# Performance work log

Measured on AMD Instinct MI355X. Metric: run time of the kernel, lower is better.

## Reference

```python
import jax, jax.numpy as jnp
import numpy as np

DIM = 256
HEAD_DIM = 32
HEADS = DIM // HEAD_DIM
SHAPE = (64, 64)          # (H, W) patch grid
WS = 8                    # window size
SHIFT = 4                 # shift size (ws // 2)
SCALE = HEAD_DIM ** -0.5
WS2 = WS * WS


def _rel_indices(ws):
    # relative position index for every (query, key) pair in a window
    a = np.arange(ws)
    y1, x1, y2, x2 = np.meshgrid(a, a, a, a, indexing='ij')
    idx = (y1 - y2 + ws - 1) * (2 * ws - 1) + (x1 - x2 + ws - 1)
    return idx.reshape(ws * ws, ws * ws)  # (ws2, ws2)


def _shift_mask(shape, ws, shift):
    # region labels per patch, 9 regions from the 3x3 slice grid
    H, W = shape
    region = np.zeros((H, W), dtype=np.int32)
    slices = [slice(0, -ws), slice(-ws, -shift), slice(-shift, None)]
    num = 0
    for i in slices:
        for j in slices:
            region[i, j] = num
            num += 1
    # window-partition the region map -> (n_windows, ws2)
    nH, nW = H // ws, W // ws
    r = region.reshape(nH, ws, nW, ws).transpose(0, 2, 1, 3).reshape(nH * nW, ws * ws)
    # True where query and key come from different regions
    return (r[:, None, :] - r[:, :, None]) != 0  # (nw, ws2, ws2)


REL_IDX = jnp.asarray(_rel_indices(WS))                 # (ws2, ws2) int
MASK = jnp.asarray(_shift_mask(SHAPE, WS, SHIFT))       # (nw, ws2, ws2) bool


def _split_windows(x, ws):
    # (b, H, W, C) -> (b * nH * nW, ws*ws, C)
    b, H, W, C = x.shape
    x = x.reshape(b, H // ws, ws, W // ws, ws, C)
    x = x.transpose(0, 1, 3, 2, 4, 5)
    return x.reshape(-1, ws * ws, C)


def _merge_windows(x, shape, ws):
    # inverse of _split_windows
    H, W = shape
    nH, nW = H // ws, W // ws
    C = x.shape[-1]
    x = x.reshape(-1, nH, nW, ws, ws, C)
    x = x.transpose(0, 1, 3, 2, 4, 5)
    return x.reshape(-1, H, W, C)


def setup_inputs() -> dict:
    key = jax.random.key(0)
    ks = jax.random.split(key, 6)
    s = 0.02
    return {
        'x': jax.random.normal(ks[0], (32, SHAPE[0] * SHAPE[1], DIM), jnp.float32),
        'w_qkv': jax.random.normal(ks[1], (3 * DIM, DIM), jnp.float32) * s,
        'b_qkv': jax.random.normal(ks[2], (3 * DIM,), jnp.float32) * s,
        'w_out': jax.random.normal(ks[3], (DIM, DIM), jnp.float32) * s,
        'b_out': jax.random.normal(ks[4], (DIM,), jnp.float32) * s,
        'pos_enc': jax.random.normal(ks[5], (HEADS, (2 * WS - 1) ** 2), jnp.float32) * s,
    }


def reference(x, w_qkv, b_qkv, w_out, b_out, pos_enc):
    B, N, C = x.shape
    H, W = SHAPE
    nw = (H // WS) * (W // WS)

    xg = x.reshape(B, H, W, C)
    if SHIFT > 0:
        xg = jnp.roll(xg, (-SHIFT, -SHIFT), axis=(1, 2))
    xw = _split_windows(xg, WS)                        # (B*nw, ws2, C)

    qkv = xw @ w_qkv.T + b_qkv                         # (B*nw, ws2, 3C)
    qkv = qkv.reshape(-1, WS2, 3, HEADS, HEAD_DIM)
    q, k, v = (qkv[:, :, i].transpose(0, 2, 1, 3) for i in range(3))  # (Bn, h, ws2, hd)

    attn = jnp.einsum('bhqd,bhkd->bhqk', q, k) * SCALE  # (Bn, h, ws2, ws2)
    bias = pos_enc[:, REL_IDX]                          # (h, ws2, ws2)
    attn = attn + bias[None]

    if SHIFT > 0:
        attn = attn.reshape(B, nw, HEADS, WS2, WS2)
        attn = jnp.where(MASK[None, :, None], -jnp.inf, attn)
        attn = attn.reshape(B * nw, HEADS, WS2, WS2)

    attn = jax.nn.softmax(attn, axis=-1)
    out = jnp.einsum('bhqk,bhkd->bhqd', attn, v)        # (Bn, h, ws2, hd)
    out = out.transpose(0, 2, 1, 3).reshape(-1, WS2, C)
    out = out @ w_out.T + b_out                         # (Bn, ws2, C)

    out = _merge_windows(out, SHAPE, WS)                # (B, H, W, C)
    if SHIFT > 0:
        out = jnp.roll(out, (SHIFT, SHIFT), axis=(1, 2))
    return out.reshape(B, N, C)
```

## Files before the change

kernel.cpp:

```cpp
#include <hip/hip_runtime.h>
#include <stdint.h>


typedef short short8 __attribute__((ext_vector_type(8)));
typedef float f32x4 __attribute__((ext_vector_type(4)));

typedef __attribute__((address_space(1))) uint32_t g_u32;
typedef __attribute__((address_space(3))) uint32_t l_u32;

#define SCALE 0.17677669529663687f

__device__ __forceinline__ uint16_t f2bf(float f) {
  union { float f; uint32_t u; } c; c.f = f;
  uint32_t r = c.u + 0x7FFFu + ((c.u >> 16) & 1u);
  return (uint16_t)(r >> 16);
}

__device__ __forceinline__ void g2lds16(const void* g, void* l) {
  __builtin_amdgcn_global_load_lds((const g_u32*)g, (l_u32*)l, 16, 0, 0);
}

__global__ __launch_bounds__(256) void cvtx_kernel(const float* __restrict__ x,
                                                   uint16_t* __restrict__ xb) {
  int tid = threadIdx.x;
  int token = blockIdx.x * 8 + (tid >> 5);
  int c = (tid & 31) * 8;
  int w = token >> 6, t = token & 63;
  int b = w >> 6, wd = w & 63;
  int h = (wd >> 3) * 8 + (t >> 3);
  int xx = (wd & 7) * 8 + (t & 7);
  int src = b * 4096 + (((h + 4) & 63) << 6) + ((xx + 4) & 63);
  const float* sp = x + (size_t)src * 256 + c;
  f32x4 a = *(const f32x4*)sp;
  f32x4 d = *(const f32x4*)(sp + 4);
  short8 v;
  v[0] = (short)f2bf(a[0]); v[1] = (short)f2bf(a[1]);
  v[2] = (short)f2bf(a[2]); v[3] = (short)f2bf(a[3]);
  v[4] = (short)f2bf(d[0]); v[5] = (short)f2bf(d[1]);
  v[6] = (short)f2bf(d[2]); v[7] = (short)f2bf(d[3]);
  *(short8*)&xb[(size_t)token * 256 + c] = v;
}

__global__ __launch_bounds__(256) void cvt_kernel(const float* __restrict__ in,
                                                  uint16_t* __restrict__ out, int n) {
  int i = (blockIdx.x * 256 + threadIdx.x) * 8;
  if (i >= n) return;
  f32x4 a = *(const f32x4*)(in + i);
  f32x4 b = *(const f32x4*)(in + i + 4);
  short8 v;
  v[0] = (short)f2bf(a[0]); v[1] = (short)f2bf(a[1]);
  v[2] = (short)f2bf(a[2]); v[3] = (short)f2bf(a[3]);
  v[4] = (short)f2bf(b[0]); v[5] = (short)f2bf(b[1]);
  v[6] = (short)f2bf(b[2]); v[7] = (short)f2bf(b[3]);
  *(short8*)(out + i) = v;
}

__global__ __launch_bounds__(256) void bias_kernel(const float* __restrict__ pe,
                                                   float* __restrict__ bm) {
  int bx = blockIdx.x;
  int wd = bx >> 3, head = bx & 7;
  int hw = wd >> 3, ww = wd & 7;
  int tid = threadIdx.x;
  int kk = tid >> 2, a0 = (tid & 3) * 4;
  int jy = kk >> 3, jx = kk & 7;
  int hj = hw * 8 + jy, xj = ww * 8 + jx;
  int rj = (hj >= 60 ? 2 : (hj >= 56 ? 1 : 0)) * 3 + (xj >= 60 ? 2 : (xj >= 56 ? 1 : 0));
  float* dst = bm + (size_t)bx * 4096 + kk * 64 + a0 * 4;
  for (int aa = 0; aa < 4; ++aa) {
    int a = a0 + aa;
    f32x4 v;
#pragma unroll
    for (int ni = 0; ni < 4; ++ni) {
      int i = ni * 16 + a;
      int iy = i >> 3, ix = i & 7;
      int hi = hw * 8 + iy, xi = ww * 8 + ix;
      int ri = (hi >= 60 ? 2 : (hi >= 56 ? 1 : 0)) * 3 + (xi >= 60 ? 2 : (xi >= 56 ? 1 : 0));
      v[ni] = (ri != rj) ? -1e30f : pe[head * 225 + (iy - jy + 7) * 15 + (ix - jx + 7)];
    }
    *(f32x4*)(dst + aa * 4) = v;
  }
}

__global__ __launch_bounds__(256) void qkv_kernel(
    const uint16_t* __restrict__ xb, const uint16_t* __restrict__ wq,
    const float* __restrict__ bqkv,
    uint16_t* __restrict__ qws, uint16_t* __restrict__ kws, uint16_t* __restrict__ vws) {
  __shared__ uint16_t sm[16384];
  uint16_t* As = sm;
  uint16_t* Bs = sm + 4096;
  const int tid = threadIdx.x, lane = tid & 63, wv = tid >> 6;
  const int quad = lane >> 4, l15 = lane & 15;
  const int n0 = blockIdx.x * 128;
  const int m0 = blockIdx.y * 128;

  const int c0 = wv * 2, c1 = c0 + 1;
  const uint16_t* ap0 = xb + (size_t)(m0 + c0 * 16 + (lane >> 2)) * 256 + (lane & 3) * 8;
  const uint16_t* ap1 = xb + (size_t)(m0 + c1 * 16 + (lane >> 2)) * 256 + (lane & 3) * 8;
  const uint16_t* bp0 = wq + (size_t)(n0 + c0 * 16 + (lane >> 2)) * 256 + (lane & 3) * 8;
  const uint16_t* bp1 = wq + (size_t)(n0 + c1 * 16 + (lane >> 2)) * 256 + (lane & 3) * 8;

  const int wm = (wv & 1) * 64, wn = (wv >> 1) * 64;
  f32x4 zero = {0.f, 0.f, 0.f, 0.f};
  f32x4 acc[4][4];
#pragma unroll
  for (int mi = 0; mi < 4; ++mi)
#pragma unroll
    for (int ni = 0; ni < 4; ++ni) acc[mi][ni] = zero;

  for (int ks = 0; ks < 8; ++ks) {
    int k0 = ks * 32;
    g2lds16(ap0 + k0, &As[c0 * 512]);
    g2lds16(ap1 + k0, &As[c1 * 512]);
    g2lds16(bp0 + k0, &Bs[c0 * 512]);
    g2lds16(bp1 + k0, &Bs[c1 * 512]);
    __syncthreads();
    short8 af[4], bf[4];
#pragma unroll
    for (int mi = 0; mi < 4; ++mi)
      af[mi] = *(const short8*)&As[(wm + mi * 16 + l15) * 32 + quad * 8];
#pragma unroll
    for (int ni = 0; ni < 4; ++ni)
      bf[ni] = *(const short8*)&Bs[(wn + ni * 16 + l15) * 32 + quad * 8];
#pragma unroll
    for (int mi = 0; mi < 4; ++mi)
#pragma unroll
      for (int ni = 0; ni < 4; ++ni)
        acc[mi][ni] = __builtin_amdgcn_mfma_f32_16x16x32_bf16(af[mi], bf[ni], acc[mi][ni], 0, 0, 0);
    __syncthreads();
  }

  float bq4[4];
#pragma unroll
  for (int ni = 0; ni < 4; ++ni) bq4[ni] = bqkv[n0 + wn + ni * 16 + l15];
  const int ng0 = n0 + wn;
  const int sct = ng0 >> 8;
  uint16_t* epi = sm + wv * 4096;

  if (sct < 2) {
#pragma unroll
    for (int mi = 0; mi < 4; ++mi)
#pragma unroll
      for (int ni = 0; ni < 4; ++ni)
#pragma unroll
        for (int r = 0; r < 4; ++r) {
          int t = mi * 16 + quad * 4 + r, n = ni * 16 + l15;
          epi[t * 64 + ((((n >> 3) ^ (t & 7)) << 3) | (n & 7))] = f2bf(acc[mi][ni][r] + bq4[ni]);
        }
    uint16_t* dst = (sct == 0) ? qws : kws;
    const int tb = m0 + wm;
#pragma unroll
    for (int cc = 0; cc < 8; ++cc) {
      int chunk = cc * 64 + lane;
      int trow = chunk >> 3, part = chunk & 7;
      short8 v = *(const short8*)&epi[trow * 64 + ((part ^ (trow & 7)) << 3)];
      int tok = tb + trow, w = tok >> 6, t = tok & 63;
      int ng = ng0 + part * 8, hd = (ng >> 5) & 7, d = ng & 31;
      *(short8*)&dst[(size_t)((w * 8 + hd) * 64 + t) * 32 + d] = v;
    }
  } else {
#pragma unroll
    for (int mi = 0; mi < 4; ++mi)
#pragma unroll
      for (int ni = 0; ni < 4; ++ni)
#pragma unroll
        for (int r = 0; r < 4; ++r) {
          int t = mi * 16 + quad * 4 + r, n = ni * 16 + l15;
          epi[n * 64 + ((((t >> 3) ^ (n & 7)) << 3) | (t & 7))] = f2bf(acc[mi][ni][r] + bq4[ni]);
        }
    const int tb = m0 + wm;
#pragma unroll
    for (int cc = 0; cc < 8; ++cc) {
      int chunk = cc * 64 + lane;
      int drow = chunk >> 3, part = chunk & 7;
      short8 v = *(const short8*)&epi[drow * 64 + ((part ^ (drow & 7)) << 3)];
      int ng = ng0 + drow, hd = (ng >> 5) & 7, d = ng & 31;
      int tok = tb + part * 8, w = tok >> 6, t = tok & 63;
      *(short8*)&vws[(size_t)((w * 8 + hd) * 32 + d) * 64 + t] = v;
    }
  }
}

__global__ __launch_bounds__(256) void attn_kernel(
    const uint16_t* __restrict__ qws, const uint16_t* __restrict__ kws,
    const uint16_t* __restrict__ vws, const float* __restrict__ bm,
    uint16_t* __restrict__ ao) {
  __shared__ uint16_t P[4][4096];
  const int tid = threadIdx.x, lane = tid & 63, wv = tid >> 6;
  const int quad = lane >> 4, l15 = lane & 15;
  const int gid = blockIdx.x * 4 + wv;
  const int w = gid >> 3, head = gid & 7;
  const uint16_t* qb = qws + (size_t)(w * 8 + head) * 2048;
  const uint16_t* kb = kws + (size_t)(w * 8 + head) * 2048;
  const uint16_t* vb = vws + (size_t)(w * 8 + head) * 2048;
  const float* bmh = bm + (size_t)((w & 63) * 8 + head) * 4096;
  f32x4 zero = {0.f, 0.f, 0.f, 0.f};

  short8 ak[4], bq[4];
#pragma unroll
  for (int mi = 0; mi < 4; ++mi)
    ak[mi] = *(const short8*)&kb[(mi * 16 + l15) * 32 + quad * 8];
#pragma unroll
  for (int ni = 0; ni < 4; ++ni)
    bq[ni] = *(const short8*)&qb[(ni * 16 + l15) * 32 + quad * 8];

  f32x4 s[4][4];
#pragma unroll
  for (int mi = 0; mi < 4; ++mi)
#pragma unroll
    for (int ni = 0; ni < 4; ++ni)
      s[mi][ni] = __builtin_amdgcn_mfma_f32_16x16x32_bf16(ak[mi], bq[ni], zero, 0, 0, 0);

#pragma unroll
  for (int mi = 0; mi < 4; ++mi)
#pragma unroll
    for (int r = 0; r < 4; ++r) {
      int kk = mi * 16 + quad * 4 + r;
      f32x4 b4 = *(const f32x4*)&bmh[kk * 64 + l15 * 4];
#pragma unroll
      for (int ni = 0; ni < 4; ++ni)
        s[mi][ni][r] = s[mi][ni][r] * SCALE + b4[ni];
    }

#pragma unroll
  for (int ni = 0; ni < 4; ++ni) {
    float mx = s[0][ni][0];
#pragma unroll
    for (int mi = 0; mi < 4; ++mi)
#pragma unroll
      for (int r = 0; r < 4; ++r) mx = fmaxf(mx, s[mi][ni][r]);
    mx = fmaxf(mx, __shfl_xor(mx, 16, 64));
    mx = fmaxf(mx, __shfl_xor(mx, 32, 64));
    float sum = 0.f;
#pragma unroll
    for (int mi = 0; mi < 4; ++mi)
#pragma unroll
      for (int r = 0; r < 4; ++r) {
        float e = __expf(s[mi][ni][r] - mx);
        s[mi][ni][r] = e;
        sum += e;
      }
    sum += __shfl_xor(sum, 16, 64);
    sum += __shfl_xor(sum, 32, 64);
    float inv = 1.f / sum;
#pragma unroll
    for (int mi = 0; mi < 4; ++mi)
#pragma unroll
      for (int r = 0; r < 4; ++r) s[mi][ni][r] *= inv;
  }

  uint16_t* Pw = P[wv];
#pragma unroll
  for (int mi = 0; mi < 4; ++mi)
#pragma unroll
    for (int ni = 0; ni < 4; ++ni)
#pragma unroll
      for (int rp = 0; rp < 2; ++rp) {
        int kk = mi * 16 + quad * 4 + rp * 2;
        int q = ni * 16 + l15;
        uint32_t pk = (uint32_t)f2bf(s[mi][ni][rp * 2]) |
                      ((uint32_t)f2bf(s[mi][ni][rp * 2 + 1]) << 16);
        *(uint32_t*)&Pw[q * 64 + ((((kk >> 3) ^ (q & 7)) << 3) | (kk & 7))] = pk;
      }

  f32x4 o[4][2];
#pragma unroll
  for (int mi = 0; mi < 4; ++mi) { o[mi][0] = zero; o[mi][1] = zero; }
#pragma unroll
  for (int ki = 0; ki < 2; ++ki) {
    short8 vf0 = *(const short8*)&vb[(l15) * 64 + ki * 32 + quad * 8];
    short8 vf1 = *(const short8*)&vb[(16 + l15) * 64 + ki * 32 + quad * 8];
#pragma unroll
    for (int mi = 0; mi < 4; ++mi) {
      int q = mi * 16 + l15;
      short8 pa = *(const short8*)&Pw[q * 64 + (((ki * 4 + quad) ^ (q & 7)) << 3)];
      o[mi][0] = __builtin_amdgcn_mfma_f32_16x16x32_bf16(pa, vf0, o[mi][0], 0, 0, 0);
      o[mi][1] = __builtin_amdgcn_mfma_f32_16x16x32_bf16(pa, vf1, o[mi][1], 0, 0, 0);
    }
  }
#pragma unroll
  for (int mi = 0; mi < 4; ++mi)
#pragma unroll
    for (int ni = 0; ni < 2; ++ni)
#pragma unroll
      for (int r = 0; r < 4; ++r) {
        int t = mi * 16 + quad * 4 + r;
        ao[(size_t)(w * 64 + t) * 256 + head * 32 + ni * 16 + l15] = f2bf(o[mi][ni][r]);
      }
}

__global__ __launch_bounds__(256) void oproj_kernel(
    const uint16_t* __restrict__ aob, const uint16_t* __restrict__ wo,
    const float* __restrict__ bout, float* __restrict__ out) {
  __shared__ uint16_t sm[8192];
  uint16_t* As = sm;
  uint16_t* Bs = sm + 4096;
  const int tid = threadIdx.x, lane = tid & 63, wv = tid >> 6;
  const int quad = lane >> 4, l15 = lane & 15;
  const int n0 = blockIdx.x * 128;
  const int m0 = blockIdx.y * 128;

  const int c0 = wv * 2, c1 = c0 + 1;
  const uint16_t* ap0 = aob + (size_t)(m0 + c0 * 16 + (lane >> 2)) * 256 + (lane & 3) * 8;
  const uint16_t* ap1 = aob + (size_t)(m0 + c1 * 16 + (lane >> 2)) * 256 + (lane & 3) * 8;
  const uint16_t* bp0 = wo + (size_t)(n0 + c0 * 16 + (lane >> 2)) * 256 + (lane & 3) * 8;
  const uint16_t* bp1 = wo + (size_t)(n0 + c1 * 16 + (lane >> 2)) * 256 + (lane & 3) * 8;

  const int wm = (wv & 1) * 64, wn = (wv >> 1) * 64;
  f32x4 zero = {0.f, 0.f, 0.f, 0.f};
  f32x4 acc[4][4];
#pragma unroll
  for (int mi = 0; mi < 4; ++mi)
#pragma unroll
    for (int ni = 0; ni < 4; ++ni) acc[mi][ni] = zero;

  for (int ks = 0; ks < 8; ++ks) {
    int k0 = ks * 32;
    g2lds16(ap0 + k0, &As[c0 * 512]);
    g2lds16(ap1 + k0, &As[c1 * 512]);
    g2lds16(bp0 + k0, &Bs[c0 * 512]);
    g2lds16(bp1 + k0, &Bs[c1 * 512]);
    __syncthreads();
    short8 af[4], bf[4];
#pragma unroll
    for (int mi = 0; mi < 4; ++mi)
      af[mi] = *(const short8*)&As[(wm + mi * 16 + l15) * 32 + quad * 8];
#pragma unroll
    for (int ni = 0; ni < 4; ++ni)
      bf[ni] = *(const short8*)&Bs[(wn + ni * 16 + l15) * 32 + quad * 8];
#pragma unroll
    for (int mi = 0; mi < 4; ++mi)
#pragma unroll
      for (int ni = 0; ni < 4; ++ni)
        acc[mi][ni] = __builtin_amdgcn_mfma_f32_16x16x32_bf16(af[mi], bf[ni], acc[mi][ni], 0, 0, 0);
    __syncthreads();
  }

  float bo4[4];
#pragma unroll
  for (int ni = 0; ni < 4; ++ni) bo4[ni] = bout[n0 + wn + ni * 16 + l15];
#pragma unroll
  for (int mi = 0; mi < 4; ++mi) {
    int mb = m0 + wm + mi * 16 + quad * 4;
    int w = mb >> 6, t0 = mb & 63;
    int b = w >> 6, wd = w & 63;
    int hw2 = wd >> 3, ww2 = wd & 7;
#pragma unroll
    for (int r = 0; r < 4; ++r) {
      int t = t0 + r;
      int h = hw2 * 8 + (t >> 3), xx = ww2 * 8 + (t & 7);
      int row = (((h + 4) & 63) << 6) | ((xx + 4) & 63);
      float* op = out + ((size_t)b * 4096 + row) * 256 + n0 + wn;
#pragma unroll
      for (int ni = 0; ni < 4; ++ni) op[ni * 16 + l15] = acc[mi][ni][r] + bo4[ni];
    }
  }
}

extern "C" void kernel_launch(void* const* d_in, const int* in_sizes, int n_in,
                              void* d_out, int out_size, void* d_ws, size_t ws_size,
                              hipStream_t stream) {
  const float* x = (const float*)d_in[0];
  const float* w_qkv = (const float*)d_in[1];
  const float* b_qkv = (const float*)d_in[2];
  const float* w_out = (const float*)d_in[3];
  const float* b_out = (const float*)d_in[4];
  const float* pos_enc = (const float*)d_in[5];
  float* out = (float*)d_out;

  uint8_t* ws = (uint8_t*)d_ws;
  uint16_t* xb  = (uint16_t*)(ws);
  uint16_t* wqb = (uint16_t*)(ws + 67108864);
  uint16_t* wob = (uint16_t*)(ws + 67502080);
  float*    bmt = (float*)   (ws + 67633152);
  uint16_t* qws = (uint16_t*)(ws + 76021760);
  uint16_t* kws = (uint16_t*)(ws + 143130624);
  uint16_t* vws = (uint16_t*)(ws + 210239488);
  uint16_t* aob = xb;

  cvtx_kernel<<<16384, 256, 0, stream>>>(x, xb);
  cvt_kernel<<<96, 256, 0, stream>>>(w_qkv, wqb, 196608);
  cvt_kernel<<<32, 256, 0, stream>>>(w_out, wob, 65536);
  bias_kernel<<<512, 256, 0, stream>>>(pos_enc, bmt);
  qkv_kernel<<<dim3(6, 1024), 256, 0, stream>>>(xb, wqb, b_qkv, qws, kws, vws);
  attn_kernel<<<4096, 256, 0, stream>>>(qws, kws, vws, bmt, aob);
  oproj_kernel<<<dim3(2, 1024), 256, 0, stream>>>(aob, wob, b_out, out);
}
```

Baseline: 446.4 us.

## Fuse x shift/convert into QKV GEMM with resident A tile and swizzled LDS

The separate fp32-to-bf16 shifted-window conversion pass over x is removed. The QKV kernel now loads its 128-token fp32 slice directly, converts it and keeps the full 128x256 bf16 A tile resident in LDS, then loops over all six 128-column output tiles with double-buffered weight loads. The two weight conversion launches are merged into one, and XOR swizzling is added to the LDS layout in both GEMMs to reduce bank conflicts. In exchange the kernel uses much more LDS (80 KB), which limits occupancy, and the grid shrinks to 1024 blocks.

Result: faster. 394.7 us (-11.6%).

```diff
diff --git a/kernel.cpp b/kernel.cpp
--- a/kernel.cpp
+++ b/kernel.cpp
@@ -3,6 +3,7 @@
 
 
 typedef short short8 __attribute__((ext_vector_type(8)));
+typedef short s16x4 __attribute__((ext_vector_type(4)));
 typedef float f32x4 __attribute__((ext_vector_type(4)));
 
 typedef __attribute__((address_space(1))) uint32_t g_u32;
@@ -20,33 +21,13 @@
   __builtin_amdgcn_global_load_lds((const g_u32*)g, (l_u32*)l, 16, 0, 0);
 }
 
-__global__ __launch_bounds__(256) void cvtx_kernel(const float* __restrict__ x,
-                                                   uint16_t* __restrict__ xb) {
-  int tid = threadIdx.x;
-  int token = blockIdx.x * 8 + (tid >> 5);
-  int c = (tid & 31) * 8;
-  int w = token >> 6, t = token & 63;
-  int b = w >> 6, wd = w & 63;
-  int h = (wd >> 3) * 8 + (t >> 3);
-  int xx = (wd & 7) * 8 + (t & 7);
-  int src = b * 4096 + (((h + 4) & 63) << 6) + ((xx + 4) & 63);
-  const float* sp = x + (size_t)src * 256 + c;
-  f32x4 a = *(const f32x4*)sp;
-  f32x4 d = *(const f32x4*)(sp + 4);
-  short8 v;
-  v[0] = (short)f2bf(a[0]); v[1] = (short)f2bf(a[1]);
-  v[2] = (short)f2bf(a[2]); v[3] = (short)f2bf(a[3]);
-  v[4] = (short)f2bf(d[0]); v[5] = (short)f2bf(d[1]);
-  v[6] = (short)f2bf(d[2]); v[7] = (short)f2bf(d[3]);
-  *(short8*)&xb[(size_t)token * 256 + c] = v;
-}
-
-__global__ __launch_bounds__(256) void cvt_kernel(const float* __restrict__ in,
-                                                  uint16_t* __restrict__ out, int n) {
+__global__ __launch_bounds__(256) void cvtw_kernel(const float* __restrict__ wq,
+                                                   const float* __restrict__ wo,
+                                                   uint16_t* __restrict__ out) {
   int i = (blockIdx.x * 256 + threadIdx.x) * 8;
-  if (i >= n) return;
-  f32x4 a = *(const f32x4*)(in + i);
-  f32x4 b = *(const f32x4*)(in + i + 4);
+  const float* src = (i < 196608) ? (wq + i) : (wo + (i - 196608));
+  f32x4 a = *(const f32x4*)src;
+  f32x4 b = *(const f32x4*)(src + 4);
   short8 v;
   v[0] = (short)f2bf(a[0]); v[1] = (short)f2bf(a[1]);
   v[2] = (short)f2bf(a[2]); v[3] = (short)f2bf(a[3]);
@@ -81,102 +62,155 @@
   }
 }
 
-__global__ __launch_bounds__(256) void qkv_kernel(
-    const uint16_t* __restrict__ xb, const uint16_t* __restrict__ wq,
+__global__ __launch_bounds__(256, 2) void qkv_kernel(
+    const float* __restrict__ x, const uint16_t* __restrict__ wq,
     const float* __restrict__ bqkv,
     uint16_t* __restrict__ qws, uint16_t* __restrict__ kws, uint16_t* __restrict__ vws) {
-  __shared__ uint16_t sm[16384];
+  __shared__ uint16_t sm[40960];
   uint16_t* As = sm;
-  uint16_t* Bs = sm + 4096;
+  uint16_t* Bs = sm + 32768;
   const int tid = threadIdx.x, lane = tid & 63, wv = tid >> 6;
   const int quad = lane >> 4, l15 = lane & 15;
-  const int n0 = blockIdx.x * 128;
-  const int m0 = blockIdx.y * 128;
-
-  const int c0 = wv * 2, c1 = c0 + 1;
-  const uint16_t* ap0 = xb + (size_t)(m0 + c0 * 16 + (lane >> 2)) * 256 + (lane & 3) * 8;
-  const uint16_t* ap1 = xb + (size_t)(m0 + c1 * 16 + (lane >> 2)) * 256 + (lane & 3) * 8;
-  const uint16_t* bp0 = wq + (size_t)(n0 + c0 * 16 + (lane >> 2)) * 256 + (lane & 3) * 8;
-  const uint16_t* bp1 = wq + (size_t)(n0 + c1 * 16 + (lane >> 2)) * 256 + (lane & 3) * 8;
-
+  const int m0 = blockIdx.x * 128;
+
+  {
+    const int rl = tid >> 3;
+    const int cg = tid & 7;
+    for (int pass = 0; pass < 4; ++pass) {
+      int row = pass * 32 + rl;
+      int token = m0 + row;
+      int w = token >> 6, t = token & 63;
+      int b = w >> 6, wd = w & 63;
+      int h = (wd >> 3) * 8 + (t >> 3);
+      int xx = (wd & 7) * 8 + (t & 7);
+      const float* sp = x + (size_t)(b * 4096 + (((h + 4) & 63) << 6) + ((xx + 4) & 63)) * 256;
+      int psw = (row >> 1) & 3;
+#pragma unroll
+      for (int j = 0; j < 4; ++j) {
+        int c0 = cg * 8 + j * 64;
+        f32x4 a = *(const f32x4*)(sp + c0);
+        f32x4 d = *(const f32x4*)(sp + c0 + 4);
+        short8 v;
+        v[0] = (short)f2bf(a[0]); v[1] = (short)f2bf(a[1]);
+        v[2] = (short)f2bf(a[2]); v[3] = (short)f2bf(a[3]);
+        v[4] = (short)f2bf(d[0]); v[5] = (short)f2bf(d[1]);
+        v[6] = (short)f2bf(d[2]); v[7] = (short)f2bf(d[3]);
+        int ks = c0 >> 5, g = (c0 >> 3) & 3;
+        *(short8*)&As[(ks * 128 + row) * 32 + (g ^ psw) * 8] = v;
+      }
+    }
+  }
+
+  const int c0s = wv * 2, c1s = c0s + 1;
+  const int perm = ((lane & 3) ^ ((lane >> 3) & 3)) * 8;
   const int wm = (wv & 1) * 64, wn = (wv >> 1) * 64;
+  const int fsw = (quad ^ ((l15 >> 1) & 3)) * 8;
+  const int tb = m0 + wm;
+  uint16_t* epi = &Bs[wv * 2048];
   f32x4 zero = {0.f, 0.f, 0.f, 0.f};
-  f32x4 acc[4][4];
-#pragma unroll
-  for (int mi = 0; mi < 4; ++mi)
-#pragma unroll
-    for (int ni = 0; ni < 4; ++ni) acc[mi][ni] = zero;
-
-  for (int ks = 0; ks < 8; ++ks) {
-    int k0 = ks * 32;
-    g2lds16(ap0 + k0, &As[c0 * 512]);
-    g2lds16(ap1 + k0, &As[c1 * 512]);
-    g2lds16(bp0 + k0, &Bs[c0 * 512]);
-    g2lds16(bp1 + k0, &Bs[c1 * 512]);
+
+  __syncthreads();
+
+  for (int nt = 0; nt < 6; ++nt) {
+    const int n0 = nt * 128;
+    const uint16_t* bp0 = wq + (size_t)(n0 + c0s * 16 + (lane >> 2)) * 256 + perm;
+    const uint16_t* bp1 = wq + (size_t)(n0 + c1s * 16 + (lane >> 2)) * 256 + perm;
+    g2lds16(bp0, &Bs[c0s * 512]);
+    g2lds16(bp1, &Bs[c1s * 512]);
+
+    f32x4 acc[4][4];
+#pragma unroll
+    for (int mi = 0; mi < 4; ++mi)
+#pragma unroll
+      for (int ni = 0; ni < 4; ++ni) acc[mi][ni] = zero;
+
     __syncthreads();
-    short8 af[4], bf[4];
-#pragma unroll
-    for (int mi = 0; mi < 4; ++mi)
-      af[mi] = *(const short8*)&As[(wm + mi * 16 + l15) * 32 + quad * 8];
-#pragma unroll
-    for (int ni = 0; ni < 4; ++ni)
-      bf[ni] = *(const short8*)&Bs[(wn + ni * 16 + l15) * 32 + quad * 8];
-#pragma unroll
-    for (int mi = 0; mi < 4; ++mi)
+
+    for (int ks = 0; ks < 8; ++ks) {
+      int buf = (ks & 1) * 4096;
+      if (ks < 7) {
+        int nbuf = 4096 - buf;
+        g2lds16(bp0 + (ks + 1) * 32, &Bs[nbuf + c0s * 512]);
+        g2lds16(bp1 + (ks + 1) * 32, &Bs[nbuf + c1s * 512]);
+      }
+      short8 af[4], bf[4];
+#pragma unroll
+      for (int mi = 0; mi < 4; ++mi)
+        af[mi] = *(const short8*)&As[(ks * 128 + wm + mi * 16 + l15) * 32 + fsw];
 #pragma unroll
       for (int ni = 0; ni < 4; ++ni)
-        acc[mi][ni] = __builtin_amdgcn_mfma_f32_16x16x32_bf16(af[mi], bf[ni], acc[mi][ni], 0, 0, 0);
+        bf[ni] = *(const short8*)&Bs[buf + (wn + ni * 16 + l15) * 32 + fsw];
+#pragma unroll
+      for (int mi = 0; mi < 4; ++mi)
+#pragma unroll
+        for (int ni = 0; ni < 4; ++ni)
+          acc[mi][ni] = __builtin_amdgcn_mfma_f32_16x16x32_bf16(af[mi], bf[ni], acc[mi][ni], 0, 0, 0);
+      __syncthreads();
+    }
+
+    float bq4[4];
+#pragma unroll
+    for (int ni = 0; ni < 4; ++ni) bq4[ni] = bqkv[n0 + wn + ni * 16 + l15];
+    const int ng0 = n0 + wn;
+    const int sct = ng0 >> 8;
+
+    if (sct < 2) {
+      uint16_t* dst = (sct == 0) ? qws : kws;
+      for (int half = 0; half < 2; ++half) {
+#pragma unroll
+        for (int mi2 = 0; mi2 < 2; ++mi2) {
+          int mi = half * 2 + mi2;
+#pragma unroll
+          for (int ni = 0; ni < 4; ++ni)
+#pragma unroll
+            for (int r = 0; r < 4; ++r) {
+              int t = mi * 16 + quad * 4 + r, tl = t & 31;
+              int n = ni * 16 + l15;
+              epi[tl * 64 + ((((n >> 3) ^ (t & 7)) << 3) | (n & 7))] =
+                  f2bf(acc[mi][ni][r] + bq4[ni]);
+            }
+        }
+#pragma unroll
+        for (int cc = 0; cc < 4; ++cc) {
+          int chunk = cc * 64 + lane;
+          int trl = chunk >> 3, part = chunk & 7;
+          int t = half * 32 + trl;
+          short8 v = *(const short8*)&epi[trl * 64 + ((part ^ (t & 7)) << 3)];
+          int tok = tb + t, w = tok >> 6, tt = tok & 63;
+          int ng = ng0 + part * 8, hd = (ng >> 5) & 7, d = ng & 31;
+          *(short8*)&dst[(size_t)((w * 8 + hd) * 64 + tt) * 32 + d] = v;
+        }
+      }
+    } else {
+      for (int half = 0; half < 2; ++half) {
+#pragma unroll
+        for (int ni2 = 0; ni2 < 2; ++ni2) {
+          int ni = half * 2 + ni2;
+          int n = ni * 16 + l15, nl = n & 31;
+#pragma unroll
+          for (int mi = 0; mi < 4; ++mi) {
+            int t0 = mi * 16 + quad * 4;
+            s16x4 pv;
+            pv[0] = (short)f2bf(acc[mi][ni][0] + bq4[ni]);
+            pv[1] = (short)f2bf(acc[mi][ni][1] + bq4[ni]);
+            pv[2] = (short)f2bf(acc[mi][ni][2] + bq4[ni]);
+            pv[3] = (short)f2bf(acc[mi][ni][3] + bq4[ni]);
+            *(s16x4*)&epi[nl * 64 + ((((t0 >> 3) ^ (n & 7)) << 3) | (t0 & 7))] = pv;
+          }
+        }
+#pragma unroll
+        for (int cc = 0; cc < 4; ++cc) {
+          int chunk = cc * 64 + lane;
+          int drl = chunk >> 3, part = chunk & 7;
+          int dr = half * 32 + drl;
+          short8 v = *(const short8*)&epi[drl * 64 + ((part ^ (dr & 7)) << 3)];
+          int ng = ng0 + dr, hd = (ng >> 5) & 7, d = ng & 31;
+          int tok = tb + part * 8, w = tok >> 6, t = tok & 63;
+          *(short8*)&vws[(size_t)((w * 8 + hd) * 32 + d) * 64 + t] = v;
+        }
+      }
+    }
     __syncthreads();
-  }
-
-  float bq4[4];
-#pragma unroll
-  for (int ni = 0; ni < 4; ++ni) bq4[ni] = bqkv[n0 + wn + ni * 16 + l15];
-  const int ng0 = n0 + wn;
-  const int sct = ng0 >> 8;
-  uint16_t* epi = sm + wv * 4096;
-
-  if (sct < 2) {
-#pragma unroll
-    for (int mi = 0; mi < 4; ++mi)
-#pragma unroll
-      for (int ni = 0; ni < 4; ++ni)
-#pragma unroll
-        for (int r = 0; r < 4; ++r) {
-          int t = mi * 16 + quad * 4 + r, n = ni * 16 + l15;
-          epi[t * 64 + ((((n >> 3) ^ (t & 7)) << 3) | (n & 7))] = f2bf(acc[mi][ni][r] + bq4[ni]);
-        }
-    uint16_t* dst = (sct == 0) ? qws : kws;
-    const int tb = m0 + wm;
-#pragma unroll
-    for (int cc = 0; cc < 8; ++cc) {
-      int chunk = cc * 64 + lane;
-      int trow = chunk >> 3, part = chunk & 7;
-      short8 v = *(const short8*)&epi[trow * 64 + ((part ^ (trow & 7)) << 3)];
-      int tok = tb + trow, w = tok >> 6, t = tok & 63;
-      int ng = ng0 + part * 8, hd = (ng >> 5) & 7, d = ng & 31;
-      *(short8*)&dst[(size_t)((w * 8 + hd) * 64 + t) * 32 + d] = v;
-    }
-  } else {
-#pragma unroll
-    for (int mi = 0; mi < 4; ++mi)
-#pragma unroll
-      for (int ni = 0; ni < 4; ++ni)
-#pragma unroll
-        for (int r = 0; r < 4; ++r) {
-          int t = mi * 16 + quad * 4 + r, n = ni * 16 + l15;
-          epi[n * 64 + ((((t >> 3) ^ (n & 7)) << 3) | (t & 7))] = f2bf(acc[mi][ni][r] + bq4[ni]);
-        }
-    const int tb = m0 + wm;
-#pragma unroll
-    for (int cc = 0; cc < 8; ++cc) {
-      int chunk = cc * 64 + lane;
-      int drow = chunk >> 3, part = chunk & 7;
-      short8 v = *(const short8*)&epi[drow * 64 + ((part ^ (drow & 7)) << 3)];
-      int ng = ng0 + drow, hd = (ng >> 5) & 7, d = ng & 31;
-      int tok = tb + part * 8, w = tok >> 6, t = tok & 63;
-      *(short8*)&vws[(size_t)((w * 8 + hd) * 32 + d) * 64 + t] = v;
-    }
   }
 }
 
@@ -300,10 +334,12 @@
   const int m0 = blockIdx.y * 128;
 
   const int c0 = wv * 2, c1 = c0 + 1;
-  const uint16_t* ap0 = aob + (size_t)(m0 + c0 * 16 + (lane >> 2)) * 256 + (lane & 3) * 8;
-  const uint16_t* ap1 = aob + (size_t)(m0 + c1 * 16 + (lane >> 2)) * 256 + (lane & 3) * 8;
-  const uint16_t* bp0 = wo + (size_t)(n0 + c0 * 16 + (lane >> 2)) * 256 + (lane & 3) * 8;
-  const uint16_t* bp1 = wo + (size_t)(n0 + c1 * 16 + (lane >> 2)) * 256 + (lane & 3) * 8;
+  const int perm = ((lane & 3) ^ ((lane >> 3) & 3)) * 8;
+  const int fsw = (quad ^ ((l15 >> 1) & 3)) * 8;
+  const uint16_t* ap0 = aob + (size_t)(m0 + c0 * 16 + (lane >> 2)) * 256 + perm;
+  const uint16_t* ap1 = aob + (size_t)(m0 + c1 * 16 + (lane >> 2)) * 256 + perm;
+  const uint16_t* bp0 = wo + (size_t)(n0 + c0 * 16 + (lane >> 2)) * 256 + perm;
+  const uint16_t* bp1 = wo + (size_t)(n0 + c1 * 16 + (lane >> 2)) * 256 + perm;
 
   const int wm = (wv & 1) * 64, wn = (wv >> 1) * 64;
   f32x4 zero = {0.f, 0.f, 0.f, 0.f};
@@ -323,10 +359,10 @@
     short8 af[4], bf[4];
 #pragma unroll
     for (int mi = 0; mi < 4; ++mi)
-      af[mi] = *(const short8*)&As[(wm + mi * 16 + l15) * 32 + quad * 8];
+      af[mi] = *(const short8*)&As[(wm + mi * 16 + l15) * 32 + fsw];
 #pragma unroll
     for (int ni = 0; ni < 4; ++ni)
-      bf[ni] = *(const short8*)&Bs[(wn + ni * 16 + l15) * 32 + quad * 8];
+      bf[ni] = *(const short8*)&Bs[(wn + ni * 16 + l15) * 32 + fsw];
 #pragma unroll
     for (int mi = 0; mi < 4; ++mi)
 #pragma unroll
@@ -368,20 +404,17 @@
   float* out = (float*)d_out;
 
   uint8_t* ws = (uint8_t*)d_ws;
-  uint16_t* xb  = (uint16_t*)(ws);
+  uint16_t* aob = (uint16_t*)(ws);
   uint16_t* wqb = (uint16_t*)(ws + 67108864);
   uint16_t* wob = (uint16_t*)(ws + 67502080);
   float*    bmt = (float*)   (ws + 67633152);
   uint16_t* qws = (uint16_t*)(ws + 76021760);
   uint16_t* kws = (uint16_t*)(ws + 143130624);
   uint16_t* vws = (uint16_t*)(ws + 210239488);
-  uint16_t* aob = xb;
-
-  cvtx_kernel<<<16384, 256, 0, stream>>>(x, xb);
-  cvt_kernel<<<96, 256, 0, stream>>>(w_qkv, wqb, 196608);
-  cvt_kernel<<<32, 256, 0, stream>>>(w_out, wob, 65536);
+
+  cvtw_kernel<<<128, 256, 0, stream>>>(w_qkv, w_out, wqb);
   bias_kernel<<<512, 256, 0, stream>>>(pos_enc, bmt);
-  qkv_kernel<<<dim3(6, 1024), 256, 0, stream>>>(xb, wqb, b_qkv, qws, kws, vws);
+  qkv_kernel<<<1024, 256, 0, stream>>>(x, wqb, b_qkv, qws, kws, vws);
   attn_kernel<<<4096, 256, 0, stream>>>(qws, kws, vws, bmt, aob);
   oproj_kernel<<<dim3(2, 1024), 256, 0, stream>>>(aob, wob, b_out, out);
 }
```
